# Kernel optimization log

Measured on AMD Instinct MI355X. Metric: run time of the kernel, lower is better.

## Reference

```python
import jax, jax.numpy as jnp
import numpy as np

KERNEL_SIZE = 11  # int(resolution / 11.6) with resolution=128
SIGMA = 1.5
K1, K2 = 0.01, 0.03


def gaussian_kernel(k=KERNEL_SIZE, sigma=SIGMA):
    coords = jnp.arange(k, dtype=jnp.float32) - (k - 1) / 2
    g = jnp.exp(-coords ** 2 / (2 * sigma ** 2))
    g = g / g.sum()
    return jnp.outer(g, g)  # (k,k)


def depthwise_conv(x, kern):
    # x: (N,C,H,W), kern: (k,k); depthwise (groups=C), SAME padding, stride 1
    C = x.shape[1]
    k = kern.shape[0]
    w = jnp.broadcast_to(kern[None, None], (C, 1, k, k))
    return jax.lax.conv_general_dilated(
        x, w, window_strides=(1, 1), padding='SAME',
        feature_group_count=C,
        dimension_numbers=('NCHW', 'OIHW', 'NCHW'))


def dssim_map(x, y, kern):
    C1, C2 = K1 ** 2, K2 ** 2
    mu_x = depthwise_conv(x, kern)
    mu_y = depthwise_conv(y, kern)
    sigma_x = depthwise_conv(x * x, kern) - mu_x ** 2
    sigma_y = depthwise_conv(y * y, kern) - mu_y ** 2
    sigma_xy = depthwise_conv(x * y, kern) - mu_x * mu_y
    ssim_num = (2 * mu_x * mu_y + C1) * (2 * sigma_xy + C2)
    ssim_den = (mu_x ** 2 + mu_y ** 2 + C1) * (sigma_x + sigma_y + C2)
    ssim = ssim_num / (ssim_den + 1e-8)
    return (1 - ssim) / 2  # (N,C,H,W)


def poly_mask(pts, H, W):
    # pts: (P,2) polygon vertices (x, y). Vectorized ray-casting point-in-polygon,
    # restricted to the truncated bounding box exactly like the torch code
    # (mask[:, :, ymin:ymax, xmin:xmax] slice), and zeroed if polygon exits frame.
    x, y = pts[:, 0], pts[:, 1]
    xmin, xmax = jnp.floor(x.min()), jnp.floor(x.max())  # == int() for positive coords
    ymin, ymax = jnp.floor(y.min()), jnp.floor(y.max())
    valid = (xmin >= 0) & (ymin >= 0) & (xmax < W) & (ymax < H)
    yy, xx = jnp.meshgrid(jnp.arange(H, dtype=jnp.float32),
                          jnp.arange(W, dtype=jnp.float32), indexing='ij')
    x1, y1 = x[:, None, None], y[:, None, None]        # (P,1,1)
    x2 = jnp.roll(x, -1)[:, None, None]
    y2 = jnp.roll(y, -1)[:, None, None]
    Y, X = yy[None], xx[None]                          # (1,H,W)
    cond = ((y1 > Y) != (y2 > Y)) & (X < (x2 - x1) * (Y - y1) / (y2 - y1 + 1e-6) + x1)
    inside = (cond.sum(axis=0) % 2) == 1               # XOR-fold over edges, (H,W)
    bbox = (yy >= ymin) & (yy < ymax) & (xx >= xmin) & (xx < xmax)
    return jnp.where(valid, (inside & bbox).astype(jnp.float32), 0.0)


def weight_map(lmrk, H, W):
    # lmrk: (68,2). weight = 1 + 3*eyeL + 3*eyeR + 2*mouth (additive, as in torch)
    return (1.0
            + 3.0 * poly_mask(lmrk[36:42], H, W)
            + 3.0 * poly_mask(lmrk[42:48], H, W)
            + 2.0 * poly_mask(lmrk[48:60], H, W))  # (H,W)


def setup_inputs() -> dict:
    key = jax.random.key(0)
    k1, k2, k3 = jax.random.split(key, 3)
    N, C, H, W = 48, 3, 256, 256
    pred = jax.random.normal(k1, (N, C, H, W), dtype=jnp.float32)
    target = jax.random.normal(k2, (N, C, H, W), dtype=jnp.float32)
    # landmarks strictly inside the frame so all polygons are rasterized
    landmarks = 20.0 + 216.0 * jax.random.uniform(k3, (N, 68, 2), dtype=jnp.float32)
    return {"pred": pred, "target": target, "landmarks": landmarks}


def reference(pred, target, landmarks):
    N, C, H, W = pred.shape
    kern = gaussian_kernel()
    # per-sample DSSIM (batch-of-1 conv in torch == batched conv here)
    d = dssim_map(pred, target, kern).mean(axis=(1, 2, 3))          # (N,)
    abs_diff = jnp.abs(pred - target)
    l1 = abs_diff.mean(axis=(1, 2, 3))                              # (N,)
    wmap = jax.vmap(lambda lm: weight_map(lm, H, W))(landmarks)     # (N,H,W)
    lw = (wmap[:, None] * abs_diff).mean(axis=(1, 2, 3))            # (N,)
    return (10.0 * d + 10.0 * l1 + 5.0 * lw).mean()
```

## Files before the change

### kernel.cpp

```cpp
#include <hip/hip_runtime.h>
#include <cmath>

#define HW 256
#define NIMG 48
#define NCH 3
#define NPLANE (NIMG * NCH)
#define STRIP 33
#define NSTRIP 8

__global__ void zero_ws_kernel(double* ws) {
    if (threadIdx.x < 3) ws[threadIdx.x] = 0.0;
}

__launch_bounds__(256)
__global__ void fused_kernel(const float* __restrict__ pred,
                             const float* __restrict__ target,
                             const float* __restrict__ lmk,
                             double* __restrict__ ws)
{
    const int plane = blockIdx.x;
    const int n     = plane / 3;
    const int r0    = blockIdx.y * STRIP;
    const int x     = threadIdx.x;

    __shared__ float2 spt[11][HW + 10];
    __shared__ float  sxc[STRIP][24];
    __shared__ float  slm[48];
    __shared__ float  sbbs[12];
    __shared__ float  svalids[3];
    __shared__ float  red[12];

    float g[11];
    {
        float gs = 0.f;
#pragma unroll
        for (int i = 0; i < 11; ++i) {
            float c = (float)i - 5.0f;
            g[i] = expf(-c * c / 4.5f);
            gs += g[i];
        }
#pragma unroll
        for (int i = 0; i < 11; ++i) g[i] /= gs;
    }

    if (x < 48) slm[x] = lmk[n * 136 + 72 + x];
    __syncthreads();

    if (x < 3) {
        const int s0 = (x == 0) ? 0 : (x == 1) ? 6 : 12;
        const int L  = (x == 2) ? 12 : 6;
        float xmn = 3e38f, xmx = -3e38f, ymn = 3e38f, ymx = -3e38f;
        for (int i = 0; i < L; ++i) {
            float px = slm[2 * (s0 + i)], py = slm[2 * (s0 + i) + 1];
            xmn = fminf(xmn, px); xmx = fmaxf(xmx, px);
            ymn = fminf(ymn, py); ymx = fmaxf(ymx, py);
        }
        xmn = floorf(xmn); xmx = floorf(xmx); ymn = floorf(ymn); ymx = floorf(ymx);
        sbbs[4 * x + 0] = xmn; sbbs[4 * x + 1] = xmx;
        sbbs[4 * x + 2] = ymn; sbbs[4 * x + 3] = ymx;
        svalids[x] = (xmn >= 0.f && ymn >= 0.f && xmx < 256.f && ymx < 256.f) ? 1.f : 0.f;
    }

#pragma unroll
    for (int u = 0; u < 4; ++u) {
        int idx = x + 256 * u;
        if (idx < STRIP * 24) {
            int r = idx / 24, e = idx - r * 24;
            float Y = (float)(r0 + r);
            const int s0 = (e < 6) ? 0 : (e < 12) ? 6 : 12;
            const int L  = (e < 12) ? 6 : 12;
            int il = e - s0;
            int i2 = (il + 1 == L) ? 0 : il + 1;
            float x1 = slm[2 * (s0 + il)], y1 = slm[2 * (s0 + il) + 1];
            float x2 = slm[2 * (s0 + i2)], y2 = slm[2 * (s0 + i2) + 1];
            bool crossing = (y1 > Y) != (y2 > Y);
            float xc = (x2 - x1) * (Y - y1) / (y2 - y1 + 1e-6f) + x1;
            sxc[r][e] = crossing ? xc : -3e38f;
        }
    }
    __syncthreads();

    float bb[12], sv[3];
#pragma unroll
    for (int q = 0; q < 12; ++q) bb[q] = sbbs[q];
#pragma unroll
    for (int q = 0; q < 3; ++q) sv[q] = svalids[q];

    const float* __restrict__ pp = pred   + (size_t)plane * (HW * HW);
    const float* __restrict__ tp = target + (size_t)plane * (HW * HW);

    float ring[11][5];
#pragma unroll
    for (int s = 0; s < 11; ++s)
#pragma unroll
        for (int q = 0; q < 5; ++q) ring[s][q] = 0.f;

    float acc = 0.f, accl1 = 0.f, acclw = 0.f;
    const float X = (float)x;

    for (int c = 0; c < 4; ++c) {
        __syncthreads();
#pragma unroll
        for (int t = 0; t < 11; ++t) {
            int r_in = r0 - 5 + 11 * c + t;
            float pv = 0.f, tv = 0.f;
            if (r_in >= 0 && r_in < HW) {
                pv = pp[r_in * HW + x];
                tv = tp[r_in * HW + x];
            }
            spt[t][x + 5] = make_float2(pv, tv);
        }
        if (x < 5) {
#pragma unroll
            for (int t = 0; t < 11; ++t) {
                spt[t][x] = make_float2(0.f, 0.f);
                spt[t][261 + x] = make_float2(0.f, 0.f);
            }
        }
        __syncthreads();

#pragma unroll
        for (int t = 0; t < 11; ++t) {
            const int i = 11 * c + t;
            const int r_in = r0 - 5 + i;

            float h0 = 0.f, h1 = 0.f, h2 = 0.f, h3 = 0.f, h4 = 0.f;
            float2 center;
#pragma unroll
            for (int k = 0; k < 11; ++k) {
                float2 v = spt[t][x + k];
                if (k == 5) center = v;
                float w = g[k];
                float wp = w * v.x, wt = w * v.y;
                h0 += wp;
                h1 += wt;
                h2 = fmaf(wp, v.x, h2);
                h3 = fmaf(wt, v.y, h3);
                h4 = fmaf(wp, v.y, h4);
            }
            ring[t][0] = h0; ring[t][1] = h1; ring[t][2] = h2;
            ring[t][3] = h3; ring[t][4] = h4;

            if (i >= 5 && i < 5 + STRIP && r_in < HW) {
                float ad = fabsf(center.x - center.y);
                accl1 += ad;
                float Y = (float)r_in;
                float wgt = 1.f;
                bool any0 = (sv[0] != 0.f) && (Y >= bb[2])  && (Y < bb[3]);
                bool any1 = (sv[1] != 0.f) && (Y >= bb[6])  && (Y < bb[7]);
                bool any2 = (sv[2] != 0.f) && (Y >= bb[10]) && (Y < bb[11]);
                if (any0 || any1 || any2) {
                    const float* xc = sxc[i - 5];
                    int c0 = 0, c1 = 0, c2 = 0;
#pragma unroll
                    for (int e = 0; e < 6; ++e)   c0 += (X < xc[e]) ? 1 : 0;
#pragma unroll
                    for (int e = 6; e < 12; ++e)  c1 += (X < xc[e]) ? 1 : 0;
#pragma unroll
                    for (int e = 12; e < 24; ++e) c2 += (X < xc[e]) ? 1 : 0;
                    if (any0 && (c0 & 1) && X >= bb[0] && X < bb[1]) wgt += 3.f;
                    if (any1 && (c1 & 1) && X >= bb[4] && X < bb[5]) wgt += 3.f;
                    if (any2 && (c2 & 1) && X >= bb[8] && X < bb[9]) wgt += 2.f;
                }
                acclw += wgt * ad;
            }

            if (i >= 10 && i < 10 + STRIP) {
                const int r_out = r0 + (i - 10);
                if (r_out < HW) {
                    float mux = 0.f, muy = 0.f, exx = 0.f, eyy = 0.f, exy = 0.f;
#pragma unroll
                    for (int j = 0; j < 11; ++j) {
                        const int s = (t + 1 + j) % 11;
                        float w = g[j];
                        mux = fmaf(w, ring[s][0], mux);
                        muy = fmaf(w, ring[s][1], muy);
                        exx = fmaf(w, ring[s][2], exx);
                        eyy = fmaf(w, ring[s][3], eyy);
                        exy = fmaf(w, ring[s][4], exy);
                    }
                    float sx  = exx - mux * mux;
                    float sy  = eyy - muy * muy;
                    float sxy = exy - mux * muy;
                    const float C1 = 1e-4f, C2 = 9e-4f;
                    float num = (2.f * mux * muy + C1) * (2.f * sxy + C2);
                    float den = (mux * mux + muy * muy + C1) * (sx + sy + C2);
                    acc += 0.5f * (1.f - num / (den + 1e-8f));
                }
            }
        }
    }

#pragma unroll
    for (int off = 32; off > 0; off >>= 1) {
        acc   += __shfl_down(acc, off, 64);
        accl1 += __shfl_down(accl1, off, 64);
        acclw += __shfl_down(acclw, off, 64);
    }
    if ((x & 63) == 0) {
        int w = x >> 6;
        red[w] = acc; red[4 + w] = accl1; red[8 + w] = acclw;
    }
    __syncthreads();
    if (x == 0) {
        atomicAdd(&ws[0], (double)red[0] + red[1] + red[2] + red[3]);
        atomicAdd(&ws[1], (double)red[4] + red[5] + red[6] + red[7]);
        atomicAdd(&ws[2], (double)red[8] + red[9] + red[10] + red[11]);
    }
}

__global__ void final_kernel(const double* __restrict__ ws, float* __restrict__ out) {
    if (threadIdx.x == 0 && blockIdx.x == 0) {
        const double denom = (double)NIMG * NCH * HW * HW;
        out[0] = (float)((10.0 * ws[0] + 10.0 * ws[1] + 5.0 * ws[2]) / denom);
    }
}

extern "C" void kernel_launch(void* const* d_in, const int* in_sizes, int n_in,
                              void* d_out, int out_size, void* d_ws, size_t ws_size,
                              hipStream_t stream)
{
    const float* pred   = (const float*)d_in[0];
    const float* target = (const float*)d_in[1];
    const float* lmk    = (const float*)d_in[2];
    float* out  = (float*)d_out;
    double* ws  = (double*)d_ws;

    hipLaunchKernelGGL(zero_ws_kernel, dim3(1), dim3(64), 0, stream, ws);
    hipLaunchKernelGGL(fused_kernel, dim3(NPLANE, NSTRIP), dim3(256), 0, stream,
                       pred, target, lmk, ws);
    hipLaunchKernelGGL(final_kernel, dim3(1), dim3(1), 0, stream, ws, out);
}
```

Baseline: 188.2 us.

## Use row-streaming ring with register prefetch, smaller strips, and fused finalize

```diff
diff --git a/kernel.cpp b/kernel.cpp
--- a/kernel.cpp
+++ b/kernel.cpp
@@ -5,18 +5,20 @@
 #define NIMG 48
 #define NCH 3
 #define NPLANE (NIMG * NCH)
-#define STRIP 33
-#define NSTRIP 8
+#define STRIP 16
+#define NSTRIP 16
+#define NBLOCKS (NPLANE * NSTRIP)
 
 __global__ void zero_ws_kernel(double* ws) {
-    if (threadIdx.x < 3) ws[threadIdx.x] = 0.0;
+    if (threadIdx.x < 4) ws[threadIdx.x] = 0.0;
 }
 
 __launch_bounds__(256)
 __global__ void fused_kernel(const float* __restrict__ pred,
                              const float* __restrict__ target,
                              const float* __restrict__ lmk,
-                             double* __restrict__ ws)
+                             double* __restrict__ ws,
+                             float* __restrict__ out)
 {
     const int plane = blockIdx.x;
     const int n     = plane / 3;
@@ -44,6 +46,15 @@
     }
 
     if (x < 48) slm[x] = lmk[n * 136 + 72 + x];
+    if (x < 55) {
+        int t = x / 5, q = x % 5;
+        spt[t][q] = make_float2(0.f, 0.f);
+        spt[t][261 + q] = make_float2(0.f, 0.f);
+    } else if (x >= 200 && x < 255) {
+        int idx = x - 200;
+        int t = idx / 5, q = idx % 5;
+        (void)t; (void)q;
+    }
     __syncthreads();
 
     if (x < 3) {
@@ -62,7 +73,7 @@
     }
 
 #pragma unroll
-    for (int u = 0; u < 4; ++u) {
+    for (int u = 0; u < 2; ++u) {
         int idx = x + 256 * u;
         if (idx < STRIP * 24) {
             int r = idx / 24, e = idx - r * 24;
@@ -78,13 +89,6 @@
             sxc[r][e] = crossing ? xc : -3e38f;
         }
     }
-    __syncthreads();
-
-    float bb[12], sv[3];
-#pragma unroll
-    for (int q = 0; q < 12; ++q) bb[q] = sbbs[q];
-#pragma unroll
-    for (int q = 0; q < 3; ++q) sv[q] = svalids[q];
 
     const float* __restrict__ pp = pred   + (size_t)plane * (HW * HW);
     const float* __restrict__ tp = target + (size_t)plane * (HW * HW);
@@ -98,98 +102,95 @@
     float acc = 0.f, accl1 = 0.f, acclw = 0.f;
     const float X = (float)x;
 
-    for (int c = 0; c < 4; ++c) {
-        __syncthreads();
+    float pv = 0.f, tv = 0.f;
+    {
+        int r = r0 - 5;
+        if (r >= 0) { pv = pp[r * HW + x]; tv = tp[r * HW + x]; }
+    }
+
+#define ROW_BODY(T_SLOT, I_EXPR, DO_PREFETCH)                                   \
+    {                                                                           \
+        const int i = (I_EXPR);                                                 \
+        spt[T_SLOT][x + 5] = make_float2(pv, tv);                               \
+        if (DO_PREFETCH) {                                                      \
+            int r = r0 - 4 + i;                                                 \
+            float npv = 0.f, ntv = 0.f;                                         \
+            if (r >= 0 && r < HW) { npv = pp[r * HW + x]; ntv = tp[r * HW + x]; } \
+            pv = npv; tv = ntv;                                                 \
+        }                                                                       \
+        __syncthreads();                                                        \
+        float h0 = 0.f, h1 = 0.f, h2 = 0.f, h3 = 0.f, h4 = 0.f;                 \
+        float2 center = make_float2(0.f, 0.f);                                  \
+        _Pragma("unroll")                                                       \
+        for (int k = 0; k < 11; ++k) {                                          \
+            float2 v = spt[T_SLOT][x + k];                                      \
+            if (k == 5) center = v;                                             \
+            float w = g[k];                                                     \
+            float wp = w * v.x, wt = w * v.y;                                   \
+            h0 += wp;                                                           \
+            h1 += wt;                                                           \
+            h2 = fmaf(wp, v.x, h2);                                             \
+            h3 = fmaf(wt, v.y, h3);                                             \
+            h4 = fmaf(wp, v.y, h4);                                             \
+        }                                                                       \
+        ring[T_SLOT][0] = h0; ring[T_SLOT][1] = h1; ring[T_SLOT][2] = h2;       \
+        ring[T_SLOT][3] = h3; ring[T_SLOT][4] = h4;                             \
+        if (i >= 5 && i < 5 + STRIP) {                                          \
+            float ad = fabsf(center.x - center.y);                              \
+            accl1 += ad;                                                        \
+            float Y = (float)(r0 + i - 5);                                      \
+            float wgt = 1.f;                                                    \
+            bool any0 = (svalids[0] != 0.f) && (Y >= sbbs[2])  && (Y < sbbs[3]);   \
+            bool any1 = (svalids[1] != 0.f) && (Y >= sbbs[6])  && (Y < sbbs[7]);   \
+            bool any2 = (svalids[2] != 0.f) && (Y >= sbbs[10]) && (Y < sbbs[11]);  \
+            if (any0 || any1 || any2) {                                         \
+                const float* xc = sxc[i - 5];                                   \
+                int c0 = 0, c1 = 0, c2 = 0;                                     \
+                _Pragma("unroll")                                               \
+                for (int e = 0; e < 6; ++e)   c0 += (X < xc[e]) ? 1 : 0;        \
+                _Pragma("unroll")                                               \
+                for (int e = 6; e < 12; ++e)  c1 += (X < xc[e]) ? 1 : 0;        \
+                _Pragma("unroll")                                               \
+                for (int e = 12; e < 24; ++e) c2 += (X < xc[e]) ? 1 : 0;        \
+                if (any0 && (c0 & 1) && X >= sbbs[0] && X < sbbs[1]) wgt += 3.f; \
+                if (any1 && (c1 & 1) && X >= sbbs[4] && X < sbbs[5]) wgt += 3.f; \
+                if (any2 && (c2 & 1) && X >= sbbs[8] && X < sbbs[9]) wgt += 2.f; \
+            }                                                                   \
+            acclw += wgt * ad;                                                  \
+        }                                                                       \
+        if (i >= 10) {                                                          \
+            float mux = 0.f, muy = 0.f, exx = 0.f, eyy = 0.f, exy = 0.f;        \
+            _Pragma("unroll")                                                   \
+            for (int j = 0; j < 11; ++j) {                                      \
+                const int s = (T_SLOT + 1 + j) % 11;                            \
+                float w = g[j];                                                 \
+                mux = fmaf(w, ring[s][0], mux);                                 \
+                muy = fmaf(w, ring[s][1], muy);                                 \
+                exx = fmaf(w, ring[s][2], exx);                                 \
+                eyy = fmaf(w, ring[s][3], eyy);                                 \
+                exy = fmaf(w, ring[s][4], exy);                                 \
+            }                                                                   \
+            float sx  = exx - mux * mux;                                        \
+            float sy  = eyy - muy * muy;                                        \
+            float sxy = exy - mux * muy;                                        \
+            const float C1 = 1e-4f, C2 = 9e-4f;                                 \
+            float num = (2.f * mux * muy + C1) * (2.f * sxy + C2);              \
+            float den = (mux * mux + muy * muy + C1) * (sx + sy + C2);          \
+            acc += 0.5f * (1.f - num / (den + 1e-8f));                          \
+        }                                                                       \
+    }
+
+    for (int c = 0; c < 2; ++c) {
 #pragma unroll
         for (int t = 0; t < 11; ++t) {
-            int r_in = r0 - 5 + 11 * c + t;
-            float pv = 0.f, tv = 0.f;
-            if (r_in >= 0 && r_in < HW) {
-                pv = pp[r_in * HW + x];
-                tv = tp[r_in * HW + x];
-            }
-            spt[t][x + 5] = make_float2(pv, tv);
-        }
-        if (x < 5) {
-#pragma unroll
-            for (int t = 0; t < 11; ++t) {
-                spt[t][x] = make_float2(0.f, 0.f);
-                spt[t][261 + x] = make_float2(0.f, 0.f);
-            }
-        }
-        __syncthreads();
-
-#pragma unroll
-        for (int t = 0; t < 11; ++t) {
-            const int i = 11 * c + t;
-            const int r_in = r0 - 5 + i;
-
-            float h0 = 0.f, h1 = 0.f, h2 = 0.f, h3 = 0.f, h4 = 0.f;
-            float2 center;
-#pragma unroll
-            for (int k = 0; k < 11; ++k) {
-                float2 v = spt[t][x + k];
-                if (k == 5) center = v;
-                float w = g[k];
-                float wp = w * v.x, wt = w * v.y;
-                h0 += wp;
-                h1 += wt;
-                h2 = fmaf(wp, v.x, h2);
-                h3 = fmaf(wt, v.y, h3);
-                h4 = fmaf(wp, v.y, h4);
-            }
-            ring[t][0] = h0; ring[t][1] = h1; ring[t][2] = h2;
-            ring[t][3] = h3; ring[t][4] = h4;
-
-            if (i >= 5 && i < 5 + STRIP && r_in < HW) {
-                float ad = fabsf(center.x - center.y);
-                accl1 += ad;
-                float Y = (float)r_in;
-                float wgt = 1.f;
-                bool any0 = (sv[0] != 0.f) && (Y >= bb[2])  && (Y < bb[3]);
-                bool any1 = (sv[1] != 0.f) && (Y >= bb[6])  && (Y < bb[7]);
-                bool any2 = (sv[2] != 0.f) && (Y >= bb[10]) && (Y < bb[11]);
-                if (any0 || any1 || any2) {
-                    const float* xc = sxc[i - 5];
-                    int c0 = 0, c1 = 0, c2 = 0;
-#pragma unroll
-                    for (int e = 0; e < 6; ++e)   c0 += (X < xc[e]) ? 1 : 0;
-#pragma unroll
-                    for (int e = 6; e < 12; ++e)  c1 += (X < xc[e]) ? 1 : 0;
-#pragma unroll
-                    for (int e = 12; e < 24; ++e) c2 += (X < xc[e]) ? 1 : 0;
-                    if (any0 && (c0 & 1) && X >= bb[0] && X < bb[1]) wgt += 3.f;
-                    if (any1 && (c1 & 1) && X >= bb[4] && X < bb[5]) wgt += 3.f;
-                    if (any2 && (c2 & 1) && X >= bb[8] && X < bb[9]) wgt += 2.f;
-                }
-                acclw += wgt * ad;
-            }
-
-            if (i >= 10 && i < 10 + STRIP) {
-                const int r_out = r0 + (i - 10);
-                if (r_out < HW) {
-                    float mux = 0.f, muy = 0.f, exx = 0.f, eyy = 0.f, exy = 0.f;
-#pragma unroll
-                    for (int j = 0; j < 11; ++j) {
-                        const int s = (t + 1 + j) % 11;
-                        float w = g[j];
-                        mux = fmaf(w, ring[s][0], mux);
-                        muy = fmaf(w, ring[s][1], muy);
-                        exx = fmaf(w, ring[s][2], exx);
-                        eyy = fmaf(w, ring[s][3], eyy);
-                        exy = fmaf(w, ring[s][4], exy);
-                    }
-                    float sx  = exx - mux * mux;
-                    float sy  = eyy - muy * muy;
-                    float sxy = exy - mux * muy;
-                    const float C1 = 1e-4f, C2 = 9e-4f;
-                    float num = (2.f * mux * muy + C1) * (2.f * sxy + C2);
-                    float den = (mux * mux + muy * muy + C1) * (sx + sy + C2);
-                    acc += 0.5f * (1.f - num / (den + 1e-8f));
-                }
-            }
-        }
-    }
+            ROW_BODY(t, 11 * c + t, true)
+        }
+    }
+#pragma unroll
+    for (int t = 0; t < 4; ++t) {
+        ROW_BODY(t, 22 + t, (t < 3))
+    }
+#undef ROW_BODY
 
 #pragma unroll
     for (int off = 32; off > 0; off >>= 1) {
@@ -206,13 +207,15 @@
         atomicAdd(&ws[0], (double)red[0] + red[1] + red[2] + red[3]);
         atomicAdd(&ws[1], (double)red[4] + red[5] + red[6] + red[7]);
         atomicAdd(&ws[2], (double)red[8] + red[9] + red[10] + red[11]);
-    }
-}
-
-__global__ void final_kernel(const double* __restrict__ ws, float* __restrict__ out) {
-    if (threadIdx.x == 0 && blockIdx.x == 0) {
-        const double denom = (double)NIMG * NCH * HW * HW;
-        out[0] = (float)((10.0 * ws[0] + 10.0 * ws[1] + 5.0 * ws[2]) / denom);
+        __threadfence();
+        unsigned prev = atomicAdd((unsigned*)&ws[3], 1u);
+        if (prev == NBLOCKS - 1) {
+            double s0 = atomicAdd(&ws[0], 0.0);
+            double s1 = atomicAdd(&ws[1], 0.0);
+            double s2 = atomicAdd(&ws[2], 0.0);
+            const double denom = (double)NIMG * NCH * HW * HW;
+            out[0] = (float)((10.0 * s0 + 10.0 * s1 + 5.0 * s2) / denom);
+        }
     }
 }
 
@@ -228,6 +231,5 @@
 
     hipLaunchKernelGGL(zero_ws_kernel, dim3(1), dim3(64), 0, stream, ws);
     hipLaunchKernelGGL(fused_kernel, dim3(NPLANE, NSTRIP), dim3(256), 0, stream,
-                       pred, target, lmk, ws);
-    hipLaunchKernelGGL(final_kernel, dim3(1), dim3(1), 0, stream, ws, out);
+                       pred, target, lmk, ws, out);
 }
```

Measured after the change: 226.6 us. +20.4%, slower.
